# Kernel tuning notes

Measured on AMD Instinct MI355X. Metric: run time of the kernel, lower is better.

The kernel has to match this reference:

```python
import jax, jax.numpy as jnp
import numpy as np

D_MODEL = 1024
N_HEADS = 16
HEAD_DIM = D_MODEL // N_HEADS
BATCH = 2
SEQ = 2048
MASK_FILL = -10000.0


def setup_inputs() -> dict:
    key = jax.random.key(0)
    ks = jax.random.split(key, 5)
    scale = 1.0 / np.sqrt(D_MODEL)
    return {
        "x": jax.random.normal(ks[0], (BATCH, SEQ, D_MODEL), dtype=jnp.float32),
        "w_q": jax.random.normal(ks[1], (D_MODEL, D_MODEL), dtype=jnp.float32) * scale,
        "w_k": jax.random.normal(ks[2], (D_MODEL, D_MODEL), dtype=jnp.float32) * scale,
        "w_v": jax.random.normal(ks[3], (D_MODEL, D_MODEL), dtype=jnp.float32) * scale,
        "w_o": jax.random.normal(ks[4], (D_MODEL, D_MODEL), dtype=jnp.float32) * scale,
    }


def reference(x, w_q, w_k, w_v, w_o):
    B, S, C = x.shape
    # Linear(bias=False): y = x @ W^T (torch stores W as [out, in])
    q = jnp.einsum("bsc,dc->bsd", x, w_q).reshape(B, S, N_HEADS, HEAD_DIM)
    k = jnp.einsum("bsc,dc->bsd", x, w_k).reshape(B, S, N_HEADS, HEAD_DIM)
    v = jnp.einsum("bsc,dc->bsd", x, w_v).reshape(B, S, N_HEADS, HEAD_DIM)
    # scores: [B, H, S, S]
    scores = jnp.einsum("bqhd,bkhd->bhqk", q, k) / np.sqrt(HEAD_DIM)
    causal = jnp.tril(jnp.ones((S, S), dtype=bool))
    scores = jnp.where(causal, scores, MASK_FILL)
    weights = jax.nn.softmax(scores, axis=-1)
    out = jnp.einsum("bhqk,bkhd->bqhd", weights, v).reshape(B, S, C)
    return jnp.einsum("bsc,dc->bsd", out, w_o)
```

## Files before the change

### kernel.cpp

```cpp
#include <hip/hip_runtime.h>

typedef __attribute__((ext_vector_type(8))) short bf16x8;
typedef __attribute__((ext_vector_type(4))) float floatx4;

static constexpr int SEQ    = 2048;
static constexpr int CDIM   = 1024;
static constexpr int NH     = 16;
static constexpr int HD     = 64;
static constexpr int NBATCH = 2;
static constexpr int MROWS  = NBATCH * SEQ;

static __device__ __forceinline__ short f2bf(float f) {
    union { float f; unsigned u; } x; x.f = f;
    unsigned r = x.u + 0x7fffu + ((x.u >> 16) & 1u);
    return (short)(r >> 16);
}

static __device__ __forceinline__ unsigned pack2bf(float lo, float hi) {
    return ((unsigned)(unsigned short)f2bf(hi) << 16) | (unsigned)(unsigned short)f2bf(lo);
}

static __device__ __forceinline__ floatx4 mfma16(bf16x8 a, bf16x8 b, floatx4 c) {
    return __builtin_amdgcn_mfma_f32_16x16x32_bf16(a, b, c, 0, 0, 0);
}

static __device__ __forceinline__ void gl_lds16(const short* g, short* l) {
    __builtin_amdgcn_global_load_lds(
        (const __attribute__((address_space(1))) void*)g,
        (__attribute__((address_space(3))) void*)l, 16, 0, 0);
}

__global__ void convert_all(
    const void* __restrict__ x,  const void* __restrict__ wq,
    const void* __restrict__ wk, const void* __restrict__ wv,
    const void* __restrict__ wo,
    short* __restrict__ xc,  short* __restrict__ wqc, short* __restrict__ wkc,
    short* __restrict__ wvc, short* __restrict__ woc,
    int* __restrict__ flag)
{
    const int tid = threadIdx.x;
    const unsigned short* xs = (const unsigned short*)x;
    int pl = 0;
    for (int i = tid; i < 2048; i += 256) {
        const int e = (xs[2 * i] >> 7) & 0xFF;
        if (e >= 110 && e <= 144) pl++;
    }
    #pragma unroll
    for (int off = 32; off > 0; off >>= 1) pl += __shfl_down(pl, off, 64);
    __shared__ int cnt;
    if (tid == 0) cnt = 0;
    __syncthreads();
    if ((tid & 63) == 0) atomicAdd(&cnt, pl);
    __syncthreads();
    const int f = (cnt < 1024) ? 1 : 0;
    if (blockIdx.x == 0 && blockIdx.y == 0 && tid == 0) *flag = f;

    const int y = blockIdx.y;
    const void* src = (y == 0) ? x  : (y == 1) ? wq : (y == 2) ? wk : (y == 3) ? wv : wo;
    short*      dst = (y == 0) ? xc : (y == 1) ? wqc : (y == 2) ? wkc : (y == 3) ? wvc : woc;
    const int n4 = (y == 0) ? (MROWS * CDIM / 4) : (CDIM * CDIM / 4);

    const int stride = gridDim.x * blockDim.x;
    for (int i = blockIdx.x * blockDim.x + tid; i < n4; i += stride) {
        if (f) {
            const float4 v = ((const float4*)src)[i];
            ((uint2*)dst)[i] = make_uint2(pack2bf(v.x, v.y), pack2bf(v.z, v.w));
        } else {
            ((uint2*)dst)[i] = ((const uint2*)src)[i];
        }
    }
}

__global__ __launch_bounds__(256) void gemm_bt128(
    const short* __restrict__ A,
    const short* __restrict__ W0, const short* __restrict__ W1, const short* __restrict__ W2,
    void* __restrict__ C0, void* __restrict__ C1, void* __restrict__ C2,
    short* __restrict__ VT, const int* __restrict__ flag)
{
    const int m0  = blockIdx.x * 128;
    const int sel = blockIdx.y >> 3;
    const int n0  = (blockIdx.y & 7) * 128;
    const short* W = (sel == 0) ? W0 : ((sel == 1) ? W1 : W2);
    void*        C = (sel == 0) ? C0 : ((sel == 1) ? C1 : C2);
    const bool f32out = (flag != nullptr) && (*flag != 0);
    const bool vtout  = (sel == 2) && (VT != nullptr);

    __shared__ __align__(16) short ta[128 * 32];
    __shared__ __align__(16) short tb[128 * 32];

    const int tid  = threadIdx.x;
    const int lane = tid & 63;
    const int wave = tid >> 6;
    const int quad = lane >> 4;
    const int l16  = lane & 15;
    const int wm   = (wave >> 1) * 64;
    const int wn   = (wave & 1) * 64;

    floatx4 acc[4][4];
    #pragma unroll
    for (int i = 0; i < 4; i++)
        #pragma unroll
        for (int j = 0; j < 4; j++)
            acc[i][j] = 0.0f;

    const int sr = lane >> 2;
    const int sc = (lane & 3) * 8;
    const short* Ab = A + (size_t)(m0 + 32 * wave + sr) * CDIM + sc;
    const short* Wb = W + (size_t)(n0 + 32 * wave + sr) * CDIM + sc;
    short* ta0 = ta + (32 * wave) * 32;
    short* tb0 = tb + (32 * wave) * 32;

    for (int k0 = 0; k0 < CDIM; k0 += 32) {
        __syncthreads();
        gl_lds16(Ab + k0, ta0);
        gl_lds16(Ab + 16 * CDIM + k0, ta0 + 16 * 32);
        gl_lds16(Wb + k0, tb0);
        gl_lds16(Wb + 16 * CDIM + k0, tb0 + 16 * 32);
        __syncthreads();

        bf16x8 af[4], bw[4];
        #pragma unroll
        for (int i = 0; i < 4; i++)
            af[i] = *(const bf16x8*)(ta + (wm + i * 16 + l16) * 32 + quad * 8);
        #pragma unroll
        for (int j = 0; j < 4; j++)
            bw[j] = *(const bf16x8*)(tb + (wn + j * 16 + l16) * 32 + quad * 8);
        #pragma unroll
        for (int i = 0; i < 4; i++)
            #pragma unroll
            for (int j = 0; j < 4; j++)
                acc[i][j] = mfma16(af[i], bw[j], acc[i][j]);
    }

    #pragma unroll
    for (int i = 0; i < 4; i++) {
        #pragma unroll
        for (int j = 0; j < 4; j++) {
            const int row0 = m0 + wm + i * 16 + quad * 4;
            const int col  = n0 + wn + j * 16 + l16;
            if (vtout) {
                const int bb  = row0 >> 11;
                const int key = row0 & 2047;
                const size_t idx = ((size_t)(bb * 1024 + col)) * 2048 + key;
                *(uint2*)(VT + idx) = make_uint2(pack2bf(acc[i][j][0], acc[i][j][1]),
                                                 pack2bf(acc[i][j][2], acc[i][j][3]));
            } else if (f32out) {
                float* cp = (float*)C + (size_t)row0 * CDIM + col;
                #pragma unroll
                for (int r = 0; r < 4; r++)
                    cp[(size_t)r * CDIM] = acc[i][j][r];
            } else {
                short* cp = (short*)C + (size_t)row0 * CDIM + col;
                #pragma unroll
                for (int r = 0; r < 4; r++)
                    cp[(size_t)r * CDIM] = f2bf(acc[i][j][r]);
            }
        }
    }
}

__global__ __launch_bounds__(256, 3) void attn_t(
    const short* __restrict__ Q, const short* __restrict__ K,
    const short* __restrict__ VT, short* __restrict__ O)
{
    const int h = blockIdx.x;
    const int b = blockIdx.y;
    const int z = blockIdx.z;
    const int u = z & 7, g = z >> 3;
    const int qt = (g == 0) ? (31 - u) : (g == 1) ? u : (g == 2) ? (23 - u) : (8 + u);
    const int nkt = (qt >> 1) + 1;

    const int tid  = threadIdx.x;
    const int lane = tid & 63;
    const int wave = tid >> 6;
    const int quad = lane >> 4;
    const int l16  = lane & 15;

    __shared__ __align__(16) short Kt[128][72];
    __shared__ __align__(16) short Vt[64][136];
    __shared__ __align__(16) short Pl[4][16][136];

    const int rowBase = b * SEQ;
    const int colH    = h * HD;
    const int qg      = qt * 64 + wave * 16 + l16;

    bf16x8 qb0, qb1;
    {
        const short* qp = Q + (size_t)(rowBase + qg) * CDIM + colH + quad * 8;
        qb0 = *(const bf16x8*)qp;
        qb1 = *(const bf16x8*)(qp + 32);
    }

    floatx4 o[4];
    #pragma unroll
    for (int nd = 0; nd < 4; nd++) o[nd] = 0.0f;
    float l_part = 0.0f;

    const int kk = tid >> 1;
    const int kd = (tid & 1) * 32;
    const short* kg = K + (size_t)(rowBase + kk) * CDIM + colH + kd;
    const int sd = tid >> 2;
    const int sk = (tid & 3) * 32;
    const short* vg = VT + ((size_t)(b * NH + h) * HD + sd) * SEQ + sk;

    uint4 ka_0 = *(const uint4*)(kg);
    uint4 ka_1 = *(const uint4*)(kg + 8);
    uint4 ka_2 = *(const uint4*)(kg + 16);
    uint4 ka_3 = *(const uint4*)(kg + 24);
    uint4 va_0 = *(const uint4*)(vg);
    uint4 va_1 = *(const uint4*)(vg + 8);
    uint4 va_2 = *(const uint4*)(vg + 16);
    uint4 va_3 = *(const uint4*)(vg + 24);

    for (int kt = 0; kt < nkt; kt++) {
        __syncthreads();
        *(uint4*)&Kt[kk][kd]      = ka_0;
        *(uint4*)&Kt[kk][kd + 8]  = ka_1;
        *(uint4*)&Kt[kk][kd + 16] = ka_2;
        *(uint4*)&Kt[kk][kd + 24] = ka_3;
        *(uint4*)&Vt[sd][sk]      = va_0;
        *(uint4*)&Vt[sd][sk + 8]  = va_1;
        *(uint4*)&Vt[sd][sk + 16] = va_2;
        *(uint4*)&Vt[sd][sk + 24] = va_3;
        __syncthreads();

        if (kt + 1 < nkt) {
            const short* kn = kg + (size_t)(kt + 1) * 128 * CDIM;
            const short* vn = vg + (kt + 1) * 128;
            ka_0 = *(const uint4*)(kn);
            ka_1 = *(const uint4*)(kn + 8);
            ka_2 = *(const uint4*)(kn + 16);
            ka_3 = *(const uint4*)(kn + 24);
            va_0 = *(const uint4*)(vn);
            va_1 = *(const uint4*)(vn + 8);
            va_2 = *(const uint4*)(vn + 16);
            va_3 = *(const uint4*)(vn + 24);
        }

        const int key0 = kt * 128;
        const bool masked = (kt == nkt - 1);

        #pragma unroll
        for (int ms = 0; ms < 8; ms++) {
            const short* kp = &Kt[ms * 16 + l16][quad * 8];
            bf16x8 ka0 = *(const bf16x8*)kp;
            bf16x8 ka1 = *(const bf16x8*)(kp + 32);
            floatx4 s = {0.f, 0.f, 0.f, 0.f};
            s = mfma16(ka0, qb0, s);
            s = mfma16(ka1, qb1, s);
            float p[4];
            #pragma unroll
            for (int r = 0; r < 4; r++) {
                float e = __expf(s[r] * 0.125f);
                if (masked && (key0 + ms * 16 + quad * 4 + r > qg)) e = 0.0f;
                p[r] = e;
                l_part += e;
            }
            *(uint2*)&Pl[wave][l16][ms * 16 + quad * 4] =
                make_uint2(pack2bf(p[0], p[1]), pack2bf(p[2], p[3]));
        }

        #pragma unroll
        for (int kc = 0; kc < 4; kc++) {
            const bf16x8 pb = *(const bf16x8*)&Pl[wave][l16][kc * 32 + quad * 8];
            #pragma unroll
            for (int nd = 0; nd < 4; nd++) {
                const bf16x8 va = *(const bf16x8*)&Vt[nd * 16 + l16][kc * 32 + quad * 8];
                o[nd] = mfma16(va, pb, o[nd]);
            }
        }
    }

    float l = l_part;
    l += __shfl_xor(l, 16, 64);
    l += __shfl_xor(l, 32, 64);
    const float inv = 1.0f / l;

    short* op = O + (size_t)(rowBase + qg) * CDIM + colH;
    #pragma unroll
    for (int nd = 0; nd < 4; nd++) {
        *(uint2*)(op + nd * 16 + quad * 4) =
            make_uint2(pack2bf(o[nd][0] * inv, o[nd][1] * inv),
                       pack2bf(o[nd][2] * inv, o[nd][3] * inv));
    }
}

extern "C" void kernel_launch(void* const* d_in, const int* in_sizes, int n_in,
                              void* d_out, int out_size, void* d_ws, size_t ws_size,
                              hipStream_t stream)
{
    const void* x  = d_in[0];
    const void* wq = d_in[1];
    const void* wk = d_in[2];
    const void* wv = d_in[3];
    const void* wo = d_in[4];

    int* flag = (int*)d_ws;
    short* w = (short*)((char*)d_ws + 256);
    const int ME  = 1024 * 1024;
    short* Wqc = w;
    short* Wkc = w + 1 * ME;
    short* Wvc = w + 2 * ME;
    short* Woc = w + 3 * ME;
    short* Xc  = w + 4 * ME;
    short* Qb  = w + 8 * ME;
    short* Kb  = w + 12 * ME;
    short* VTb = w + 16 * ME;
    short* Ob  = Xc;

    dim3 blk(256);
    convert_all<<<dim3(512, 5), blk, 0, stream>>>(
        x, wq, wk, wv, wo, Xc, Wqc, Wkc, Wvc, Woc, flag);

    gemm_bt128<<<dim3(MROWS / 128, 24), blk, 0, stream>>>(
        Xc, Wqc, Wkc, Wvc, Qb, Kb, nullptr, VTb, nullptr);
    attn_t<<<dim3(NH, NBATCH, SEQ / 64), blk, 0, stream>>>(Qb, Kb, VTb, Ob);
    gemm_bt128<<<dim3(MROWS / 128, 8), blk, 0, stream>>>(
        Ob, Woc, Woc, Woc, d_out, d_out, d_out, nullptr, flag);
}
```

Measured before the change: 202.3 us.

## Widen GEMM K-tile with XOR-swizzled LDS and process two query tiles per attention block

The projection GEMM now stages 64-wide K slices instead of 32, using an XOR swizzle on the LDS column index to avoid bank conflicts, which halves the number of barrier-separated load iterations. The attention kernel now has each block handle two 64-row query tiles (128 rows) against each loaded K/V tile, halving the K/V global and LDS staging traffic per query row. The grid shrinks to 16 z-blocks, and occupancy drops from 3 to 2 blocks per CU to fit the extra registers. Causal balancing changes to pairing tiles from opposite ends of the sequence, but the fewer, larger blocks may load-balance less evenly.

```diff
diff --git a/kernel.cpp b/kernel.cpp
--- a/kernel.cpp
+++ b/kernel.cpp
@@ -85,8 +85,8 @@
     const bool f32out = (flag != nullptr) && (*flag != 0);
     const bool vtout  = (sel == 2) && (VT != nullptr);
 
-    __shared__ __align__(16) short ta[128 * 32];
-    __shared__ __align__(16) short tb[128 * 32];
+    __shared__ __align__(16) short ta[128 * 64];
+    __shared__ __align__(16) short tb[128 * 64];
 
     const int tid  = threadIdx.x;
     const int lane = tid & 63;
@@ -103,33 +103,41 @@
         for (int j = 0; j < 4; j++)
             acc[i][j] = 0.0f;
 
-    const int sr = lane >> 2;
-    const int sc = (lane & 3) * 8;
-    const short* Ab = A + (size_t)(m0 + 32 * wave + sr) * CDIM + sc;
-    const short* Wb = W + (size_t)(n0 + 32 * wave + sr) * CDIM + sc;
-    short* ta0 = ta + (32 * wave) * 32;
-    short* tb0 = tb + (32 * wave) * 32;
-
-    for (int k0 = 0; k0 < CDIM; k0 += 32) {
+    const int sr8 = lane >> 3;
+    const int ug  = ((lane & 7) ^ sr8) * 8;
+    const short* Ab = A + (size_t)(m0 + 32 * wave + sr8) * CDIM + ug;
+    const short* Wb = W + (size_t)(n0 + 32 * wave + sr8) * CDIM + ug;
+    short* ta0 = ta + (32 * wave) * 64;
+    short* tb0 = tb + (32 * wave) * 64;
+
+    for (int k0 = 0; k0 < CDIM; k0 += 64) {
         __syncthreads();
-        gl_lds16(Ab + k0, ta0);
-        gl_lds16(Ab + 16 * CDIM + k0, ta0 + 16 * 32);
-        gl_lds16(Wb + k0, tb0);
-        gl_lds16(Wb + 16 * CDIM + k0, tb0 + 16 * 32);
+        gl_lds16(Ab + k0,             ta0);
+        gl_lds16(Ab +  8 * CDIM + k0, ta0 +  8 * 64);
+        gl_lds16(Ab + 16 * CDIM + k0, ta0 + 16 * 64);
+        gl_lds16(Ab + 24 * CDIM + k0, ta0 + 24 * 64);
+        gl_lds16(Wb + k0,             tb0);
+        gl_lds16(Wb +  8 * CDIM + k0, tb0 +  8 * 64);
+        gl_lds16(Wb + 16 * CDIM + k0, tb0 + 16 * 64);
+        gl_lds16(Wb + 24 * CDIM + k0, tb0 + 24 * 64);
         __syncthreads();
 
-        bf16x8 af[4], bw[4];
-        #pragma unroll
-        for (int i = 0; i < 4; i++)
-            af[i] = *(const bf16x8*)(ta + (wm + i * 16 + l16) * 32 + quad * 8);
-        #pragma unroll
-        for (int j = 0; j < 4; j++)
-            bw[j] = *(const bf16x8*)(tb + (wn + j * 16 + l16) * 32 + quad * 8);
-        #pragma unroll
-        for (int i = 0; i < 4; i++)
+        #pragma unroll
+        for (int kc = 0; kc < 2; kc++) {
+            const int pu = (((kc * 4 + quad) ^ (l16 & 7))) * 8;
+            bf16x8 af[4], bw[4];
+            #pragma unroll
+            for (int i = 0; i < 4; i++)
+                af[i] = *(const bf16x8*)(ta + (wm + i * 16 + l16) * 64 + pu);
             #pragma unroll
             for (int j = 0; j < 4; j++)
-                acc[i][j] = mfma16(af[i], bw[j], acc[i][j]);
+                bw[j] = *(const bf16x8*)(tb + (wn + j * 16 + l16) * 64 + pu);
+            #pragma unroll
+            for (int i = 0; i < 4; i++)
+                #pragma unroll
+                for (int j = 0; j < 4; j++)
+                    acc[i][j] = mfma16(af[i], bw[j], acc[i][j]);
+        }
     }
 
     #pragma unroll
@@ -159,16 +167,15 @@
     }
 }
 
-__global__ __launch_bounds__(256, 3) void attn_t(
+__global__ __launch_bounds__(256, 2) void attn_t(
     const short* __restrict__ Q, const short* __restrict__ K,
     const short* __restrict__ VT, short* __restrict__ O)
 {
     const int h = blockIdx.x;
     const int b = blockIdx.y;
-    const int z = blockIdx.z;
-    const int u = z & 7, g = z >> 3;
-    const int qt = (g == 0) ? (31 - u) : (g == 1) ? u : (g == 2) ? (23 - u) : (8 + u);
-    const int nkt = (qt >> 1) + 1;
+    const int z  = blockIdx.z;
+    const int qt2 = (z < 8) ? (15 - z) : (z - 8);
+    const int nkt = qt2 + 1;
 
     const int tid  = threadIdx.x;
     const int lane = tid & 63;
@@ -182,19 +189,23 @@
 
     const int rowBase = b * SEQ;
     const int colH    = h * HD;
-    const int qg      = qt * 64 + wave * 16 + l16;
-
-    bf16x8 qb0, qb1;
+    const int qgA     = qt2 * 128 + wave * 16 + l16;
+    const int qgB     = qgA + 64;
+
+    bf16x8 qa0, qa1, qc0, qc1;
     {
-        const short* qp = Q + (size_t)(rowBase + qg) * CDIM + colH + quad * 8;
-        qb0 = *(const bf16x8*)qp;
-        qb1 = *(const bf16x8*)(qp + 32);
-    }
-
-    floatx4 o[4];
-    #pragma unroll
-    for (int nd = 0; nd < 4; nd++) o[nd] = 0.0f;
-    float l_part = 0.0f;
+        const short* qp = Q + (size_t)(rowBase + qgA) * CDIM + colH + quad * 8;
+        qa0 = *(const bf16x8*)qp;
+        qa1 = *(const bf16x8*)(qp + 32);
+        const short* qp2 = qp + (size_t)64 * CDIM;
+        qc0 = *(const bf16x8*)qp2;
+        qc1 = *(const bf16x8*)(qp2 + 32);
+    }
+
+    floatx4 oA[4], oB[4];
+    #pragma unroll
+    for (int nd = 0; nd < 4; nd++) { oA[nd] = 0.0f; oB[nd] = 0.0f; }
+    float lA = 0.0f, lB = 0.0f;
 
     const int kk = tid >> 1;
     const int kd = (tid & 1) * 32;
@@ -243,45 +254,79 @@
         #pragma unroll
         for (int ms = 0; ms < 8; ms++) {
             const short* kp = &Kt[ms * 16 + l16][quad * 8];
-            bf16x8 ka0 = *(const bf16x8*)kp;
-            bf16x8 ka1 = *(const bf16x8*)(kp + 32);
+            bf16x8 k0 = *(const bf16x8*)kp;
+            bf16x8 k1 = *(const bf16x8*)(kp + 32);
             floatx4 s = {0.f, 0.f, 0.f, 0.f};
-            s = mfma16(ka0, qb0, s);
-            s = mfma16(ka1, qb1, s);
+            s = mfma16(k0, qa0, s);
+            s = mfma16(k1, qa1, s);
             float p[4];
             #pragma unroll
             for (int r = 0; r < 4; r++) {
                 float e = __expf(s[r] * 0.125f);
-                if (masked && (key0 + ms * 16 + quad * 4 + r > qg)) e = 0.0f;
+                if (masked && (key0 + ms * 16 + quad * 4 + r > qgA)) e = 0.0f;
                 p[r] = e;
-                l_part += e;
+                lA += e;
             }
             *(uint2*)&Pl[wave][l16][ms * 16 + quad * 4] =
                 make_uint2(pack2bf(p[0], p[1]), pack2bf(p[2], p[3]));
         }
-
         #pragma unroll
         for (int kc = 0; kc < 4; kc++) {
             const bf16x8 pb = *(const bf16x8*)&Pl[wave][l16][kc * 32 + quad * 8];
             #pragma unroll
             for (int nd = 0; nd < 4; nd++) {
                 const bf16x8 va = *(const bf16x8*)&Vt[nd * 16 + l16][kc * 32 + quad * 8];
-                o[nd] = mfma16(va, pb, o[nd]);
-            }
-        }
-    }
-
-    float l = l_part;
-    l += __shfl_xor(l, 16, 64);
-    l += __shfl_xor(l, 32, 64);
-    const float inv = 1.0f / l;
-
-    short* op = O + (size_t)(rowBase + qg) * CDIM + colH;
+                oA[nd] = mfma16(va, pb, oA[nd]);
+            }
+        }
+
+        #pragma unroll
+        for (int ms = 0; ms < 8; ms++) {
+            const short* kp = &Kt[ms * 16 + l16][quad * 8];
+            bf16x8 k0 = *(const bf16x8*)kp;
+            bf16x8 k1 = *(const bf16x8*)(kp + 32);
+            floatx4 s = {0.f, 0.f, 0.f, 0.f};
+            s = mfma16(k0, qc0, s);
+            s = mfma16(k1, qc1, s);
+            float p[4];
+            #pragma unroll
+            for (int r = 0; r < 4; r++) {
+                float e = __expf(s[r] * 0.125f);
+                if (masked && (key0 + ms * 16 + quad * 4 + r > qgB)) e = 0.0f;
+                p[r] = e;
+                lB += e;
+            }
+            *(uint2*)&Pl[wave][l16][ms * 16 + quad * 4] =
+                make_uint2(pack2bf(p[0], p[1]), pack2bf(p[2], p[3]));
+        }
+        #pragma unroll
+        for (int kc = 0; kc < 4; kc++) {
+            const bf16x8 pb = *(const bf16x8*)&Pl[wave][l16][kc * 32 + quad * 8];
+            #pragma unroll
+            for (int nd = 0; nd < 4; nd++) {
+                const bf16x8 va = *(const bf16x8*)&Vt[nd * 16 + l16][kc * 32 + quad * 8];
+                oB[nd] = mfma16(va, pb, oB[nd]);
+            }
+        }
+    }
+
+    lA += __shfl_xor(lA, 16, 64);
+    lA += __shfl_xor(lA, 32, 64);
+    lB += __shfl_xor(lB, 16, 64);
+    lB += __shfl_xor(lB, 32, 64);
+    const float invA = 1.0f / lA;
+    const float invB = 1.0f / lB;
+
+    short* opA = O + (size_t)(rowBase + qgA) * CDIM + colH;
+    short* opB = O + (size_t)(rowBase + qgB) * CDIM + colH;
     #pragma unroll
     for (int nd = 0; nd < 4; nd++) {
-        *(uint2*)(op + nd * 16 + quad * 4) =
-            make_uint2(pack2bf(o[nd][0] * inv, o[nd][1] * inv),
-                       pack2bf(o[nd][2] * inv, o[nd][3] * inv));
+        *(uint2*)(opA + nd * 16 + quad * 4) =
+            make_uint2(pack2bf(oA[nd][0] * invA, oA[nd][1] * invA),
+                       pack2bf(oA[nd][2] * invA, oA[nd][3] * invA));
+        *(uint2*)(opB + nd * 16 + quad * 4) =
+            make_uint2(pack2bf(oB[nd][0] * invB, oB[nd][1] * invB),
+                       pack2bf(oB[nd][2] * invB, oB[nd][3] * invB));
     }
 }
 
@@ -314,7 +359,7 @@
 
     gemm_bt128<<<dim3(MROWS / 128, 24), blk, 0, stream>>>(
         Xc, Wqc, Wkc, Wvc, Qb, Kb, nullptr, VTb, nullptr);
-    attn_t<<<dim3(NH, NBATCH, SEQ / 64), blk, 0, stream>>>(Qb, Kb, VTb, Ob);
+    attn_t<<<dim3(NH, NBATCH, SEQ / 128), blk, 0, stream>>>(Qb, Kb, VTb, Ob);
     gemm_bt128<<<dim3(MROWS / 128, 8), blk, 0, stream>>>(
         Ob, Woc, Woc, Woc, d_out, d_out, d_out, nullptr, flag);
 }
```

Result: no change. 198.7 us (-1.8%).
